# Performance work log

Measured on AMD Instinct MI355X. Metric: run time of the kernel, lower is better.

## Reference

```python
import jax, jax.numpy as jnp
import numpy as np

N_NODES = 50000
N_EDGES = 600000
N_GRAPHS = 64
D_FEAT = 128
DIM_H = 128
N_HOPS = 3
OUT_DIM = 10


def setup_inputs() -> dict:
    key = jax.random.key(0)
    ks = jax.random.split(key, 16)
    x = jax.random.normal(ks[0], (N_NODES, D_FEAT), dtype=jnp.float32)
    edge_index = jax.random.randint(ks[1], (2, N_EDGES), 0, N_NODES, dtype=jnp.int64)
    batch = jnp.sort(jax.random.randint(ks[2], (N_NODES,), 0, N_GRAPHS, dtype=jnp.int64))
    def glorot(k, shape):
        fan = shape[0] + shape[1]
        return jax.random.uniform(k, shape, jnp.float32, -1.0, 1.0) * np.sqrt(6.0 / fan)
    # GCNConv weights stored as [in, out]; Linear weights stored as [in, out]
    W1 = glorot(ks[3], (D_FEAT, DIM_H)); b1 = jnp.zeros((DIM_H,), jnp.float32)
    W2 = glorot(ks[4], (DIM_H, DIM_H)); b2 = jnp.zeros((DIM_H,), jnp.float32)
    W3 = glorot(ks[5], (DIM_H, DIM_H)); b3 = jnp.zeros((DIM_H,), jnp.float32)
    H3 = DIM_H * N_HOPS
    lin1_W = glorot(ks[6], (H3, H3)); lin1_b = jnp.zeros((H3,), jnp.float32)
    lin2_W = glorot(ks[7], (H3, OUT_DIM)); lin2_b = jnp.zeros((OUT_DIM,), jnp.float32)
    return {"x": x, "W1": W1, "b1": b1, "W2": W2, "b2": b2, "W3": W3, "b3": b3,
            "lin1_W": lin1_W, "lin1_b": lin1_b, "lin2_W": lin2_W, "lin2_b": lin2_b,
            "edge_index": edge_index, "batch": batch}


def gcn_conv(x, W, b, src, dst, n_nodes):
    # PyG GCNConv (add_self_loops=True, normalize=True):
    #   deg[i] = in-degree at target + 1 (self loop); norm = d^-1/2[src] * d^-1/2[dst]
    deg = jnp.zeros((n_nodes,), x.dtype).at[dst].add(1.0) + 1.0
    dinv = jax.lax.rsqrt(deg)
    xw = x @ W  # [N, H] transform before propagate
    coef = (dinv[src] * dinv[dst])[:, None]
    agg = jnp.zeros_like(xw).at[dst].add(xw[src] * coef)
    agg = agg + xw * (dinv * dinv)[:, None]  # self-loop messages
    return agg + b


def global_mean_pool(h, batch, n_graphs):
    sums = jax.ops.segment_sum(h, batch, num_segments=n_graphs)
    cnt = jax.ops.segment_sum(jnp.ones((h.shape[0],), h.dtype), batch, num_segments=n_graphs)
    return sums / jnp.maximum(cnt, 1.0)[:, None]


def reference(x, W1, b1, W2, b2, W3, b3, lin1_W, lin1_b, lin2_W, lin2_b, edge_index, batch):
    src, dst = edge_index[0], edge_index[1]
    n = x.shape[0]
    h1 = gcn_conv(x, W1, b1, src, dst, n)
    h2 = gcn_conv(h1, W2, b2, src, dst, n)
    h3 = gcn_conv(h2, W3, b3, src, dst, n)
    pooled = jnp.concatenate([global_mean_pool(h, batch, N_GRAPHS) for h in (h1, h2, h3)], axis=1)
    h = jax.nn.relu(pooled @ lin1_W + lin1_b)
    # dropout is identity in eval mode
    h = h @ lin2_W + lin2_b
    return (h, jax.nn.log_softmax(h, axis=1))
```

## Files before the change

kernel.cpp:

```cpp
#include <hip/hip_runtime.h>
#include <hip/hip_fp16.h>
#include <math.h>

#define N_NODES 50000
#define N_EDGES 600000
#define N_GRAPHS 64
#define DFEAT 128
#define H3 384
#define OUTD 10
#define SCAN_BLOCKS 196
#define FILL_BLOCKS 2344
#define POOL_CHUNKS 16
#define APAD 136
#define GHALF 3125

typedef _Float16 f16x8 __attribute__((ext_vector_type(8)));
typedef float f32x4 __attribute__((ext_vector_type(4)));
typedef float f32x2 __attribute__((ext_vector_type(2)));

__global__ __launch_bounds__(256) void k_deg(const int* __restrict__ ei, int* __restrict__ deg,
                                             int* __restrict__ rank) {
    int e = blockIdx.x * 256 + threadIdx.x;
    if (e >= N_EDGES) return;
    int dst = ei[N_EDGES + e];
    rank[e] = atomicAdd(&deg[dst], 1);
}

__global__ __launch_bounds__(256) void k_part(const int* __restrict__ deg, int* __restrict__ part) {
    __shared__ int red[256];
    int tid = threadIdx.x;
    int i = blockIdx.x * 256 + tid;
    red[tid] = (i < N_NODES) ? deg[i] : 0;
    __syncthreads();
    for (int s = 128; s > 0; s >>= 1) {
        if (tid < s) red[tid] += red[tid + s];
        __syncthreads();
    }
    if (tid == 0) part[blockIdx.x] = red[0];
}

__global__ __launch_bounds__(256) void k_offsets(const int* __restrict__ deg, const int* __restrict__ part,
                                                 int* __restrict__ offs, float* __restrict__ dinv) {
    __shared__ int pbuf[256];
    __shared__ int buf[256];
    int tid = threadIdx.x;
    int pv = (tid < SCAN_BLOCKS) ? part[tid] : 0;
    pbuf[tid] = pv;
    __syncthreads();
    for (int d = 1; d < 256; d <<= 1) {
        int t = (tid >= d) ? pbuf[tid - d] : 0;
        __syncthreads();
        pbuf[tid] += t;
        __syncthreads();
    }
    int base = (blockIdx.x > 0) ? pbuf[blockIdx.x - 1] : 0;
    int i = blockIdx.x * 256 + tid;
    int v = (i < N_NODES) ? deg[i] : 0;
    buf[tid] = v;
    __syncthreads();
    for (int d = 1; d < 256; d <<= 1) {
        int t = (tid >= d) ? buf[tid - d] : 0;
        __syncthreads();
        buf[tid] += t;
        __syncthreads();
    }
    if (i < N_NODES) {
        int excl = base + buf[tid] - v;
        offs[i] = excl;
        dinv[i] = rsqrtf((float)v + 1.0f);
        if (i == N_NODES - 1) offs[N_NODES] = base + buf[tid];
    }
}

__global__ __launch_bounds__(256) void k_fill_prep(const int* __restrict__ ei, const int* __restrict__ offs,
                                                   const int* __restrict__ rank, const float* __restrict__ dinv,
                                                   unsigned int* __restrict__ epack,
                                                   const float* __restrict__ W1, const float* __restrict__ W2,
                                                   const float* __restrict__ W3, _Float16* __restrict__ Wt,
                                                   float* __restrict__ pooled) {
    int b = blockIdx.x;
    if (b < FILL_BLOCKS) {
        int e = b * 256 + threadIdx.x;
        if (e >= N_EDGES) return;
        int s = ei[e];
        int t = ei[N_EDGES + e];
        unsigned short dh = __half_as_ushort(__float2half(dinv[s]));
        epack[offs[t] + rank[e]] = (unsigned int)s | ((unsigned int)dh << 16);
    } else if (b < FILL_BLOCKS + 192) {
        int idx = (b - FILL_BLOCKS) * 256 + threadIdx.x;
        int l = idx >> 14, r = idx & 16383;
        const float* W = (l == 0) ? W1 : (l == 1) ? W2 : W3;
        int k = r >> 7, n = r & 127;
        Wt[l * 16384 + n * 128 + k] = (_Float16)W[k * 128 + n];
    } else {
        int idx = (b - FILL_BLOCKS - 192) * 256 + threadIdx.x;
        if (idx < N_GRAPHS * H3) pooled[idx] = 0.0f;
    }
}

template <bool A_FP16>
__global__ __launch_bounds__(256) void gemm_mfma(const void* __restrict__ Aptr, const _Float16* __restrict__ Wt,
                                                 unsigned char* __restrict__ T, int M) {
    __shared__ _Float16 Ws[128 * APAD];
    int tid = threadIdx.x;
    int base = blockIdx.x * 64;
    for (int c = tid; c < 2048; c += 256) {
        int n = c >> 4, c8 = (c & 15) << 3;
        *(f16x8*)&Ws[n * APAD + c8] = *(const f16x8*)&Wt[n * 128 + c8];
    }
    int wave = tid >> 6, lane = tid & 63;
    int m = lane & 15, quad = lane >> 4;
    int gr = base + wave * 16 + m;
    int grc = (gr < M) ? gr : (M - 1);
    f16x8 areg[4];
    if (A_FP16) {
        const _Float16* A = (const _Float16*)Aptr;
#pragma unroll
        for (int kc = 0; kc < 4; ++kc)
            areg[kc] = *(const f16x8*)&A[(size_t)grc * 128 + kc * 32 + quad * 8];
    } else {
        const float* A = (const float*)Aptr;
#pragma unroll
        for (int kc = 0; kc < 4; ++kc) {
            const float* src = A + (size_t)grc * 128 + kc * 32 + quad * 8;
            float4 v0 = *(const float4*)(src);
            float4 v1 = *(const float4*)(src + 4);
            f16x8 h;
            h[0] = (_Float16)v0.x; h[1] = (_Float16)v0.y; h[2] = (_Float16)v0.z; h[3] = (_Float16)v0.w;
            h[4] = (_Float16)v1.x; h[5] = (_Float16)v1.y; h[6] = (_Float16)v1.z; h[7] = (_Float16)v1.w;
            areg[kc] = h;
        }
    }
    __syncthreads();
    f32x4 acc[8];
#pragma unroll
    for (int ct = 0; ct < 8; ++ct) acc[ct] = (f32x4){0.f, 0.f, 0.f, 0.f};
#pragma unroll
    for (int kc = 0; kc < 4; ++kc) {
#pragma unroll
        for (int ct = 0; ct < 8; ++ct) {
            f16x8 b = *(const f16x8*)&Ws[(ct * 16 + m) * APAD + kc * 32 + quad * 8];
            acc[ct] = __builtin_amdgcn_mfma_f32_16x16x32_f16(b, areg[kc], acc[ct], 0, 0, 0);
        }
    }
    if (gr < M) {
#pragma unroll
        for (int ct = 0; ct < 8; ++ct) {
            int col = ct * 16 + quad * 4;
            int p = __builtin_amdgcn_cvt_pk_fp8_f32(acc[ct][0], acc[ct][1], 0, false);
            p     = __builtin_amdgcn_cvt_pk_fp8_f32(acc[ct][2], acc[ct][3], p, true);
            *(int*)(T + (size_t)gr * 128 + col) = p;
        }
    }
}

__global__ __launch_bounds__(256) void gather_agg(const unsigned int* __restrict__ T32,
                                                  const unsigned int* __restrict__ epack,
                                                  const int* __restrict__ offs,
                                                  const float* __restrict__ dinv, const float* __restrict__ bias,
                                                  __half2* __restrict__ H2) {
    int b = blockIdx.x;
    int half = (b >= GHALF) ? 1 : 0;
    int nb = b - half * GHALF;
    int q = threadIdx.x >> 4;
    int l16 = threadIdx.x & 15;
    int node = nb * 16 + q;
    int cbase = half * 16 + l16;
    unsigned su = T32[(size_t)node * 32 + cbase];
    float di = dinv[node];
    float4 b4 = *(const float4*)(bias + half * 64 + l16 * 4);
    float a0 = 0.f, a1 = 0.f, a2 = 0.f, a3 = 0.f;
    int lo = offs[node], hi = offs[node + 1];
    int hm1 = hi - 1;
    for (int e0 = lo; e0 < hi; e0 += 16) {
        unsigned p[16];
#pragma unroll
        for (int j = 0; j < 16; ++j) p[j] = epack[min(e0 + j, hm1)];
        unsigned u[16];
#pragma unroll
        for (int j = 0; j < 16; ++j) u[j] = T32[(size_t)(p[j] & 0xffffu) * 32 + cbase];
#pragma unroll
        for (int j = 0; j < 16; ++j) {
            float c = (e0 + j < hi) ? __half2float(__ushort_as_half((unsigned short)(p[j] >> 16))) : 0.0f;
            f32x2 tl = __builtin_amdgcn_cvt_pk_f32_fp8(u[j], false);
            f32x2 th = __builtin_amdgcn_cvt_pk_f32_fp8(u[j], true);
            a0 += tl.x * c; a1 += tl.y * c; a2 += th.x * c; a3 += th.y * c;
        }
    }
    f32x2 sl = __builtin_amdgcn_cvt_pk_f32_fp8(su, false), sh = __builtin_amdgcn_cvt_pk_f32_fp8(su, true);
    float dd = di * di;
    float r0 = di * a0 + sl.x * dd + b4.x;
    float r1 = di * a1 + sl.y * dd + b4.y;
    float r2 = di * a2 + sh.x * dd + b4.z;
    float r3 = di * a3 + sh.y * dd + b4.w;
    __half2 ha = __floats2half2_rn(r0, r1);
    __half2 hb = __floats2half2_rn(r2, r3);
    uint2 st = make_uint2(*(unsigned*)&ha, *(unsigned*)&hb);
    *(uint2*)&H2[(size_t)node * 64 + half * 32 + l16 * 2] = st;
}

__global__ __launch_bounds__(256) void pool_kernel(const __half2* __restrict__ H0,
                                                   const __half2* __restrict__ H1,
                                                   const __half2* __restrict__ H2buf,
                                                   const int* __restrict__ batch,
                                                   float* __restrict__ pooled) {
    __shared__ int bounds[2];
    __shared__ float2 red[256];
    int g = blockIdx.x >> 4;
    int chunk = blockIdx.x & (POOL_CHUNKS - 1);
    int tid = threadIdx.x;
    int d2 = tid & 63, sub = tid >> 6;
    if (tid < 2) {
        int target = g + tid;
        int lo = 0, hi = N_NODES;
        while (lo < hi) {
            int mid = (lo + hi) >> 1;
            if (batch[mid] < target) lo = mid + 1; else hi = mid;
        }
        bounds[tid] = lo;
    }
    __syncthreads();
    int lo = bounds[0], hi = bounds[1];
    int n = hi - lo;
    int per = (n + POOL_CHUNKS - 1) / POOL_CHUNKS;
    int s = lo + chunk * per;
    int e = s + per; if (e > hi) e = hi;
    const __half2* Hs[3] = {H0, H1, H2buf};
    for (int l = 0; l < 3; ++l) {
        const __half2* H = Hs[l];
        float ax = 0.0f, ay = 0.0f;
        for (int r = s + sub; r < e; r += 4) {
            float2 v = __half22float2(H[(size_t)r * 64 + d2]);
            ax += v.x; ay += v.y;
        }
        red[tid] = make_float2(ax, ay);
        __syncthreads();
        if (sub == 0 && s < e) {
            float2 v0 = red[d2], v1 = red[64 + d2], v2 = red[128 + d2], v3 = red[192 + d2];
            atomicAdd(&pooled[g * H3 + l * 128 + d2 * 2],     v0.x + v1.x + v2.x + v3.x);
            atomicAdd(&pooled[g * H3 + l * 128 + d2 * 2 + 1], v0.y + v1.y + v2.y + v3.y);
        }
        __syncthreads();
    }
}

__global__ __launch_bounds__(384) void mlp_kernel(const float* __restrict__ pooled,
                                                  const int* __restrict__ batch,
                                                  const float* __restrict__ l1W, const float* __restrict__ l1b,
                                                  const float* __restrict__ l2W, const float* __restrict__ l2b,
                                                  float* __restrict__ out) {
    __shared__ float p[H3];
    __shared__ float hid[H3];
    __shared__ float o10[OUTD];
    __shared__ int bnd[2];
    int g = blockIdx.x, tid = threadIdx.x;
    if (tid < 2) {
        int target = g + tid;
        int lo = 0, hi = N_NODES;
        while (lo < hi) {
            int mid = (lo + hi) >> 1;
            if (batch[mid] < target) lo = mid + 1; else hi = mid;
        }
        bnd[tid] = lo;
    }
    __syncthreads();
    float inv = 1.0f / fmaxf((float)(bnd[1] - bnd[0]), 1.0f);
    p[tid] = pooled[g * H3 + tid] * inv;
    __syncthreads();
    float acc = l1b[tid];
    for (int k = 0; k < H3; ++k) acc += p[k] * l1W[k * H3 + tid];
    hid[tid] = fmaxf(acc, 0.0f);
    __syncthreads();
    if (tid < OUTD) {
        float o = l2b[tid];
        for (int k = 0; k < H3; ++k) o += hid[k] * l2W[k * OUTD + tid];
        o10[tid] = o;
        out[g * OUTD + tid] = o;
    }
    __syncthreads();
    if (tid == 0) {
        float m = o10[0];
        for (int j = 1; j < OUTD; ++j) m = fmaxf(m, o10[j]);
        float s = 0.0f;
        for (int j = 0; j < OUTD; ++j) s += expf(o10[j] - m);
        float lse = m + logf(s);
        for (int j = 0; j < OUTD; ++j) out[N_GRAPHS * OUTD + g * OUTD + j] = o10[j] - lse;
    }
}

extern "C" void kernel_launch(void* const* d_in, const int* in_sizes, int n_in,
                              void* d_out, int out_size, void* d_ws, size_t ws_size,
                              hipStream_t stream) {
    const float* x      = (const float*)d_in[0];
    const float* W1     = (const float*)d_in[1];
    const float* b1     = (const float*)d_in[2];
    const float* W2     = (const float*)d_in[3];
    const float* b2     = (const float*)d_in[4];
    const float* W3     = (const float*)d_in[5];
    const float* b3     = (const float*)d_in[6];
    const float* lin1_W = (const float*)d_in[7];
    const float* lin1_b = (const float*)d_in[8];
    const float* lin2_W = (const float*)d_in[9];
    const float* lin2_b = (const float*)d_in[10];
    const int* edge_index = (const int*)d_in[11];
    const int* batch      = (const int*)d_in[12];

    char* ws = (char*)d_ws;
    auto alloc = [&](size_t bytes) -> void* {
        void* p = (void*)ws;
        ws += (bytes + 255) & ~(size_t)255;
        return p;
    };
    int*   deg    = (int*)  alloc((size_t)N_NODES * 4);
    int*   part   = (int*)  alloc((size_t)SCAN_BLOCKS * 4);
    int*   offs   = (int*)  alloc((size_t)(N_NODES + 1) * 4);
    int*   rank   = (int*)  alloc((size_t)N_EDGES * 4);
    float* dinv   = (float*)alloc((size_t)N_NODES * 4);
    unsigned int* epack = (unsigned int*)alloc((size_t)N_EDGES * 4);
    unsigned char* T = (unsigned char*)alloc((size_t)N_NODES * 128);
    __half* Hbuf[3];
    for (int l = 0; l < 3; ++l) Hbuf[l] = (__half*)alloc((size_t)N_NODES * 128 * 2);
    _Float16* Wt  = (_Float16*)alloc((size_t)3 * 128 * 128 * 2);
    float* pooled = (float*)alloc((size_t)N_GRAPHS * H3 * 4);

    hipMemsetAsync(deg, 0, (size_t)N_NODES * 4, stream);
    k_deg<<<(N_EDGES + 255) / 256, 256, 0, stream>>>(edge_index, deg, rank);
    k_part<<<SCAN_BLOCKS, 256, 0, stream>>>(deg, part);
    k_offsets<<<SCAN_BLOCKS, 256, 0, stream>>>(deg, part, offs, dinv);
    k_fill_prep<<<FILL_BLOCKS + 192 + 96, 256, 0, stream>>>(edge_index, offs, rank, dinv, epack,
                                                            W1, W2, W3, Wt, pooled);

    const float* bs[3] = {b1, b2, b3};
    for (int l = 0; l < 3; ++l) {
        if (l == 0)
            gemm_mfma<false><<<(N_NODES + 63) / 64, 256, 0, stream>>>(x, Wt, T, N_NODES);
        else
            gemm_mfma<true><<<(N_NODES + 63) / 64, 256, 0, stream>>>(Hbuf[l - 1], Wt + (size_t)l * 16384, T, N_NODES);
        gather_agg<<<2 * GHALF, 256, 0, stream>>>((const unsigned int*)T, epack, offs, dinv, bs[l], (__half2*)Hbuf[l]);
    }
    pool_kernel<<<N_GRAPHS * POOL_CHUNKS, 256, 0, stream>>>((const __half2*)Hbuf[0], (const __half2*)Hbuf[1],
                                                            (const __half2*)Hbuf[2], batch, pooled);
    mlp_kernel<<<N_GRAPHS, 384, 0, stream>>>(pooled, batch, lin1_W, lin1_b, lin2_W, lin2_b, (float*)d_out);
}
```

Before: 275.3 us.

## Fuse pooling with MLP via last-block counter and widen gather rows

Pooling and the MLP head now run in one kernel. A per-graph atomic counter picks the last finishing chunk block, which runs the MLP, then resets the pooled sums and the counter for the next call. This removes one kernel launch and its dependency gap. The gather kernel now has 32 lanes cover a full 128-column row per node, instead of splitting each row across two halves in separate blocks, so each edge index is loaded once per node rather than twice. In exchange, 384-wide MLP work runs on 256-thread blocks with a loop, on only 64 blocks at the tail.

```diff
diff --git a/kernel.cpp b/kernel.cpp
--- a/kernel.cpp
+++ b/kernel.cpp
@@ -12,7 +12,7 @@
 #define FILL_BLOCKS 2344
 #define POOL_CHUNKS 16
 #define APAD 136
-#define GHALF 3125
+#define ZTAIL (N_GRAPHS * H3 + N_GRAPHS)
 
 typedef _Float16 f16x8 __attribute__((ext_vector_type(8)));
 typedef float f32x4 __attribute__((ext_vector_type(4)));
@@ -77,7 +77,7 @@
                                                    unsigned int* __restrict__ epack,
                                                    const float* __restrict__ W1, const float* __restrict__ W2,
                                                    const float* __restrict__ W3, _Float16* __restrict__ Wt,
-                                                   float* __restrict__ pooled) {
+                                                   float* __restrict__ pooled, int* __restrict__ cnt) {
     int b = blockIdx.x;
     if (b < FILL_BLOCKS) {
         int e = b * 256 + threadIdx.x;
@@ -95,6 +95,7 @@
     } else {
         int idx = (b - FILL_BLOCKS - 192) * 256 + threadIdx.x;
         if (idx < N_GRAPHS * H3) pooled[idx] = 0.0f;
+        else if (idx < ZTAIL) cnt[idx - N_GRAPHS * H3] = 0;
     }
 }
 
@@ -159,16 +160,12 @@
                                                   const int* __restrict__ offs,
                                                   const float* __restrict__ dinv, const float* __restrict__ bias,
                                                   __half2* __restrict__ H2) {
-    int b = blockIdx.x;
-    int half = (b >= GHALF) ? 1 : 0;
-    int nb = b - half * GHALF;
-    int q = threadIdx.x >> 4;
-    int l16 = threadIdx.x & 15;
-    int node = nb * 16 + q;
-    int cbase = half * 16 + l16;
-    unsigned su = T32[(size_t)node * 32 + cbase];
+    int h = threadIdx.x >> 5;
+    int l32 = threadIdx.x & 31;
+    int node = blockIdx.x * 8 + h;
+    unsigned su = T32[(size_t)node * 32 + l32];
     float di = dinv[node];
-    float4 b4 = *(const float4*)(bias + half * 64 + l16 * 4);
+    float4 b4 = *(const float4*)(bias + l32 * 4);
     float a0 = 0.f, a1 = 0.f, a2 = 0.f, a3 = 0.f;
     int lo = offs[node], hi = offs[node + 1];
     int hm1 = hi - 1;
@@ -178,7 +175,7 @@
         for (int j = 0; j < 16; ++j) p[j] = epack[min(e0 + j, hm1)];
         unsigned u[16];
 #pragma unroll
-        for (int j = 0; j < 16; ++j) u[j] = T32[(size_t)(p[j] & 0xffffu) * 32 + cbase];
+        for (int j = 0; j < 16; ++j) u[j] = T32[(size_t)(p[j] & 0xffffu) * 32 + l32];
 #pragma unroll
         for (int j = 0; j < 16; ++j) {
             float c = (e0 + j < hi) ? __half2float(__ushort_as_half((unsigned short)(p[j] >> 16))) : 0.0f;
@@ -193,19 +190,24 @@
     float r1 = di * a1 + sl.y * dd + b4.y;
     float r2 = di * a2 + sh.x * dd + b4.z;
     float r3 = di * a3 + sh.y * dd + b4.w;
-    __half2 ha = __floats2half2_rn(r0, r1);
-    __half2 hb = __floats2half2_rn(r2, r3);
-    uint2 st = make_uint2(*(unsigned*)&ha, *(unsigned*)&hb);
-    *(uint2*)&H2[(size_t)node * 64 + half * 32 + l16 * 2] = st;
-}
-
-__global__ __launch_bounds__(256) void pool_kernel(const __half2* __restrict__ H0,
-                                                   const __half2* __restrict__ H1,
-                                                   const __half2* __restrict__ H2buf,
-                                                   const int* __restrict__ batch,
-                                                   float* __restrict__ pooled) {
+    H2[(size_t)node * 64 + l32 * 2]     = __floats2half2_rn(r0, r1);
+    H2[(size_t)node * 64 + l32 * 2 + 1] = __floats2half2_rn(r2, r3);
+}
+
+__global__ __launch_bounds__(256) void pool_mlp(const __half2* __restrict__ H0,
+                                                const __half2* __restrict__ H1,
+                                                const __half2* __restrict__ H2buf,
+                                                const int* __restrict__ batch,
+                                                float* __restrict__ pooled, int* __restrict__ cnt,
+                                                const float* __restrict__ l1W, const float* __restrict__ l1b,
+                                                const float* __restrict__ l2W, const float* __restrict__ l2b,
+                                                float* __restrict__ out) {
     __shared__ int bounds[2];
     __shared__ float2 red[256];
+    __shared__ int lastFlag;
+    __shared__ float p[H3];
+    __shared__ float hid[H3];
+    __shared__ float o10[OUTD];
     int g = blockIdx.x >> 4;
     int chunk = blockIdx.x & (POOL_CHUNKS - 1);
     int tid = threadIdx.x;
@@ -242,34 +244,24 @@
         }
         __syncthreads();
     }
-}
-
-__global__ __launch_bounds__(384) void mlp_kernel(const float* __restrict__ pooled,
-                                                  const int* __restrict__ batch,
-                                                  const float* __restrict__ l1W, const float* __restrict__ l1b,
-                                                  const float* __restrict__ l2W, const float* __restrict__ l2b,
-                                                  float* __restrict__ out) {
-    __shared__ float p[H3];
-    __shared__ float hid[H3];
-    __shared__ float o10[OUTD];
-    __shared__ int bnd[2];
-    int g = blockIdx.x, tid = threadIdx.x;
-    if (tid < 2) {
-        int target = g + tid;
-        int lo = 0, hi = N_NODES;
-        while (lo < hi) {
-            int mid = (lo + hi) >> 1;
-            if (batch[mid] < target) lo = mid + 1; else hi = mid;
-        }
-        bnd[tid] = lo;
-    }
-    __syncthreads();
-    float inv = 1.0f / fmaxf((float)(bnd[1] - bnd[0]), 1.0f);
-    p[tid] = pooled[g * H3 + tid] * inv;
-    __syncthreads();
-    float acc = l1b[tid];
-    for (int k = 0; k < H3; ++k) acc += p[k] * l1W[k * H3 + tid];
-    hid[tid] = fmaxf(acc, 0.0f);
+    __threadfence();
+    if (tid == 0) {
+        int old = atomicAdd(&cnt[g], 1);
+        lastFlag = (old == POOL_CHUNKS - 1);
+        if (lastFlag) cnt[g] = 0;
+    }
+    __syncthreads();
+    if (!lastFlag) return;
+    __threadfence();
+    float inv = 1.0f / fmaxf((float)n, 1.0f);
+    for (int k = tid; k < H3; k += 256) p[k] = pooled[g * H3 + k] * inv;
+    __syncthreads();
+    for (int k = tid; k < H3; k += 256) pooled[g * H3 + k] = 0.0f;
+    for (int j = tid; j < H3; j += 256) {
+        float acc = l1b[j];
+        for (int k = 0; k < H3; ++k) acc += p[k] * l1W[k * H3 + j];
+        hid[j] = fmaxf(acc, 0.0f);
+    }
     __syncthreads();
     if (tid < OUTD) {
         float o = l2b[tid];
@@ -281,9 +273,9 @@
     if (tid == 0) {
         float m = o10[0];
         for (int j = 1; j < OUTD; ++j) m = fmaxf(m, o10[j]);
-        float s = 0.0f;
-        for (int j = 0; j < OUTD; ++j) s += expf(o10[j] - m);
-        float lse = m + logf(s);
+        float sum = 0.0f;
+        for (int j = 0; j < OUTD; ++j) sum += expf(o10[j] - m);
+        float lse = m + logf(sum);
         for (int j = 0; j < OUTD; ++j) out[N_GRAPHS * OUTD + g * OUTD + j] = o10[j] - lse;
     }
 }
@@ -322,13 +314,14 @@
     for (int l = 0; l < 3; ++l) Hbuf[l] = (__half*)alloc((size_t)N_NODES * 128 * 2);
     _Float16* Wt  = (_Float16*)alloc((size_t)3 * 128 * 128 * 2);
     float* pooled = (float*)alloc((size_t)N_GRAPHS * H3 * 4);
+    int*   cnt    = (int*)  alloc((size_t)N_GRAPHS * 4);
 
     hipMemsetAsync(deg, 0, (size_t)N_NODES * 4, stream);
     k_deg<<<(N_EDGES + 255) / 256, 256, 0, stream>>>(edge_index, deg, rank);
     k_part<<<SCAN_BLOCKS, 256, 0, stream>>>(deg, part);
     k_offsets<<<SCAN_BLOCKS, 256, 0, stream>>>(deg, part, offs, dinv);
-    k_fill_prep<<<FILL_BLOCKS + 192 + 96, 256, 0, stream>>>(edge_index, offs, rank, dinv, epack,
-                                                            W1, W2, W3, Wt, pooled);
+    k_fill_prep<<<FILL_BLOCKS + 192 + 97, 256, 0, stream>>>(edge_index, offs, rank, dinv, epack,
+                                                            W1, W2, W3, Wt, pooled, cnt);
 
     const float* bs[3] = {b1, b2, b3};
     for (int l = 0; l < 3; ++l) {
@@ -336,9 +329,9 @@
             gemm_mfma<false><<<(N_NODES + 63) / 64, 256, 0, stream>>>(x, Wt, T, N_NODES);
         else
             gemm_mfma<true><<<(N_NODES + 63) / 64, 256, 0, stream>>>(Hbuf[l - 1], Wt + (size_t)l * 16384, T, N_NODES);
-        gather_agg<<<2 * GHALF, 256, 0, stream>>>((const unsigned int*)T, epack, offs, dinv, bs[l], (__half2*)Hbuf[l]);
-    }
-    pool_kernel<<<N_GRAPHS * POOL_CHUNKS, 256, 0, stream>>>((const __half2*)Hbuf[0], (const __half2*)Hbuf[1],
-                                                            (const __half2*)Hbuf[2], batch, pooled);
-    mlp_kernel<<<N_GRAPHS, 384, 0, stream>>>(pooled, batch, lin1_W, lin1_b, lin2_W, lin2_b, (float*)d_out);
-}
+        gather_agg<<<N_NODES / 8, 256, 0, stream>>>((const unsigned int*)T, epack, offs, dinv, bs[l], (__half2*)Hbuf[l]);
+    }
+    pool_mlp<<<N_GRAPHS * POOL_CHUNKS, 256, 0, stream>>>((const __half2*)Hbuf[0], (const __half2*)Hbuf[1],
+                                                         (const __half2*)Hbuf[2], batch, pooled, cnt,
+                                                         lin1_W, lin1_b, lin2_W, lin2_b, (float*)d_out);
+}
```

After: 369.3 us. 34.1% more time.
